# Kernel optimization log

Hardware: AMD Instinct MI355X
Metric: run time of the kernel (lower is better)

Reference implementation:

```python
import jax, jax.numpy as jnp
import numpy as np

EPS = 1e-4

def setup_inputs() -> dict:
    key = jax.random.key(0)
    x = jax.random.normal(key, (16, 256, 8192), dtype=jnp.float32)
    return {"x": x}

def reference(x):
    # x: [B, C, T]; cumulative (causal) normalization along time axis
    T = x.shape[-1]
    count = jnp.arange(1, T + 1, dtype=x.dtype).reshape(1, 1, T)
    cum_sum = jnp.cumsum(x, axis=-1)
    cum_pow_sum = jnp.cumsum(x * x, axis=-1)
    cum_mean = cum_sum / count
    cum_var = cum_pow_sum / count - cum_mean * cum_mean
    cum_std = jnp.sqrt(cum_var + EPS)
    return (x - cum_mean) / cum_std
```

## Files before the change

### kernel.cpp

```cpp
#include <hip/hip_runtime.h>

#define ROW_T   8192
#define THREADS 256
#define ITEMS   4
#define STILE   (THREADS * ITEMS)
#define NST     (ROW_T / STILE)
#define EPSV    1e-4f

__global__ __launch_bounds__(THREADS, 8)
void cumnorm_kernel(const float* __restrict__ x, float* __restrict__ out) {
    __shared__ float wbs[2][4];
    __shared__ float wbss[2][4];

    const int t    = threadIdx.x;
    const int lane = t & 63;
    const int wid  = t >> 6;

    const float* __restrict__ xr   = x   + (long long)blockIdx.x * ROW_T;
    float* __restrict__       outr = out + (long long)blockIdx.x * ROW_T;

    float carry_s = 0.f, carry_ss = 0.f;

    float4 cur = *reinterpret_cast<const float4*>(xr + t * ITEMS);
    float4 nxt;

    #pragma unroll
    for (int k = 0; k < NST; ++k) {
        if (k + 1 < NST)
            nxt = *reinterpret_cast<const float4*>(xr + (k + 1) * STILE + t * ITEMS);

        float s  = ((cur.x + cur.y) + (cur.z + cur.w));
        float ss = fmaf(cur.x, cur.x, fmaf(cur.y, cur.y,
                   fmaf(cur.z, cur.z, cur.w * cur.w)));

        float is = s, iss = ss;
        #pragma unroll
        for (int off = 1; off < 64; off <<= 1) {
            const float us  = __shfl_up(is, off);
            const float uss = __shfl_up(iss, off);
            if (lane >= off) { is += us; iss += uss; }
        }
        if (lane == 63) { wbs[k & 1][wid] = is; wbss[k & 1][wid] = iss; }
        __syncthreads();

        float cs = carry_s, css = carry_ss;
        #pragma unroll
        for (int w = 0; w < 4; ++w) {
            const float a = wbs[k & 1][w], b = wbss[k & 1][w];
            if (w < wid) { cs += a; css += b; }
            carry_s += a; carry_ss += b;
        }

        float S  = cs  + (is  - s);
        float SS = css + (iss - ss);

        const int e0 = k * STILE + t * ITEMS;
        float4 o;
        {
            const float v = cur.x; S += v; SS = fmaf(v, v, SS);
            const float inv = __builtin_amdgcn_rcpf((float)(e0 + 1));
            const float mean = S * inv;
            const float var  = fmaf(SS, inv, -(mean * mean));
            o.x = (v - mean) * __builtin_amdgcn_rsqf(var + EPSV);
        }
        {
            const float v = cur.y; S += v; SS = fmaf(v, v, SS);
            const float inv = __builtin_amdgcn_rcpf((float)(e0 + 2));
            const float mean = S * inv;
            const float var  = fmaf(SS, inv, -(mean * mean));
            o.y = (v - mean) * __builtin_amdgcn_rsqf(var + EPSV);
        }
        {
            const float v = cur.z; S += v; SS = fmaf(v, v, SS);
            const float inv = __builtin_amdgcn_rcpf((float)(e0 + 3));
            const float mean = S * inv;
            const float var  = fmaf(SS, inv, -(mean * mean));
            o.z = (v - mean) * __builtin_amdgcn_rsqf(var + EPSV);
        }
        {
            const float v = cur.w; S += v; SS = fmaf(v, v, SS);
            const float inv = __builtin_amdgcn_rcpf((float)(e0 + 4));
            const float mean = S * inv;
            const float var  = fmaf(SS, inv, -(mean * mean));
            o.w = (v - mean) * __builtin_amdgcn_rsqf(var + EPSV);
        }

        *reinterpret_cast<float4*>(outr + e0) = o;
        cur = nxt;
    }
}

extern "C" void kernel_launch(void* const* d_in, const int* in_sizes, int n_in,
                              void* d_out, int out_size, void* d_ws, size_t ws_size,
                              hipStream_t stream) {
    const float* x = (const float*)d_in[0];
    float* out = (float*)d_out;
    const int rows = out_size / ROW_T;
    cumnorm_kernel<<<rows, THREADS, 0, stream>>>(x, out);
}
```

Measured before the change: 229.4 us.

## Scan whole row in one pass with 1024-thread blocks and nontemporal stores

```diff
diff --git a/kernel.cpp b/kernel.cpp
--- a/kernel.cpp
+++ b/kernel.cpp
@@ -1,16 +1,17 @@
 #include <hip/hip_runtime.h>
 
 #define ROW_T   8192
-#define THREADS 256
-#define ITEMS   4
-#define STILE   (THREADS * ITEMS)
-#define NST     (ROW_T / STILE)
+#define THREADS 1024
+#define ITEMS   8
+#define NWAVES  (THREADS / 64)
 #define EPSV    1e-4f
+
+typedef float fvec4 __attribute__((ext_vector_type(4)));
 
 __global__ __launch_bounds__(THREADS, 8)
 void cumnorm_kernel(const float* __restrict__ x, float* __restrict__ out) {
-    __shared__ float wbs[2][4];
-    __shared__ float wbss[2][4];
+    __shared__ float wbs[NWAVES];
+    __shared__ float wbss[NWAVES];
 
     const int t    = threadIdx.x;
     const int lane = t & 63;
@@ -19,75 +20,55 @@
     const float* __restrict__ xr   = x   + (long long)blockIdx.x * ROW_T;
     float* __restrict__       outr = out + (long long)blockIdx.x * ROW_T;
 
-    float carry_s = 0.f, carry_ss = 0.f;
+    const int e0 = t * ITEMS;
 
-    float4 cur = *reinterpret_cast<const float4*>(xr + t * ITEMS);
-    float4 nxt;
+    const fvec4 va = *reinterpret_cast<const fvec4*>(xr + e0);
+    const fvec4 vb = *reinterpret_cast<const fvec4*>(xr + e0 + 4);
 
+    float s  = ((va.x + va.y) + (va.z + va.w)) + ((vb.x + vb.y) + (vb.z + vb.w));
+    float ss = fmaf(va.x, va.x, fmaf(va.y, va.y, fmaf(va.z, va.z, va.w * va.w)));
+    ss = fmaf(vb.x, vb.x, fmaf(vb.y, vb.y, fmaf(vb.z, vb.z, fmaf(vb.w, vb.w, ss))));
+
+    float is = s, iss = ss;
     #pragma unroll
-    for (int k = 0; k < NST; ++k) {
-        if (k + 1 < NST)
-            nxt = *reinterpret_cast<const float4*>(xr + (k + 1) * STILE + t * ITEMS);
+    for (int off = 1; off < 64; off <<= 1) {
+        const float us  = __shfl_up(is, off);
+        const float uss = __shfl_up(iss, off);
+        if (lane >= off) { is += us; iss += uss; }
+    }
+    if (lane == 63) { wbs[wid] = is; wbss[wid] = iss; }
+    __syncthreads();
 
-        float s  = ((cur.x + cur.y) + (cur.z + cur.w));
-        float ss = fmaf(cur.x, cur.x, fmaf(cur.y, cur.y,
-                   fmaf(cur.z, cur.z, cur.w * cur.w)));
+    float cs = 0.f, css = 0.f;
+    #pragma unroll
+    for (int w = 0; w < NWAVES; ++w) {
+        const float a = wbs[w], b = wbss[w];
+        if (w < wid) { cs += a; css += b; }
+    }
 
-        float is = s, iss = ss;
-        #pragma unroll
-        for (int off = 1; off < 64; off <<= 1) {
-            const float us  = __shfl_up(is, off);
-            const float uss = __shfl_up(iss, off);
-            if (lane >= off) { is += us; iss += uss; }
-        }
-        if (lane == 63) { wbs[k & 1][wid] = is; wbss[k & 1][wid] = iss; }
-        __syncthreads();
+    float S  = cs  + (is  - s);
+    float SS = css + (iss - ss);
 
-        float cs = carry_s, css = carry_ss;
-        #pragma unroll
-        for (int w = 0; w < 4; ++w) {
-            const float a = wbs[k & 1][w], b = wbss[k & 1][w];
-            if (w < wid) { cs += a; css += b; }
-            carry_s += a; carry_ss += b;
-        }
+    fvec4 o0, o1;
+#define CN_STEP(v, idx, dst) {                                            \
+        S += (v); SS = fmaf((v), (v), SS);                                \
+        const float inv  = __builtin_amdgcn_rcpf((float)(e0 + (idx) + 1));\
+        const float mean = S * inv;                                       \
+        const float var  = fmaf(SS, inv, -(mean * mean));                 \
+        (dst) = ((v) - mean) * __builtin_amdgcn_rsqf(var + EPSV);         \
+    }
+    CN_STEP(va.x, 0, o0.x)
+    CN_STEP(va.y, 1, o0.y)
+    CN_STEP(va.z, 2, o0.z)
+    CN_STEP(va.w, 3, o0.w)
+    CN_STEP(vb.x, 4, o1.x)
+    CN_STEP(vb.y, 5, o1.y)
+    CN_STEP(vb.z, 6, o1.z)
+    CN_STEP(vb.w, 7, o1.w)
+#undef CN_STEP
 
-        float S  = cs  + (is  - s);
-        float SS = css + (iss - ss);
-
-        const int e0 = k * STILE + t * ITEMS;
-        float4 o;
-        {
-            const float v = cur.x; S += v; SS = fmaf(v, v, SS);
-            const float inv = __builtin_amdgcn_rcpf((float)(e0 + 1));
-            const float mean = S * inv;
-            const float var  = fmaf(SS, inv, -(mean * mean));
-            o.x = (v - mean) * __builtin_amdgcn_rsqf(var + EPSV);
-        }
-        {
-            const float v = cur.y; S += v; SS = fmaf(v, v, SS);
-            const float inv = __builtin_amdgcn_rcpf((float)(e0 + 2));
-            const float mean = S * inv;
-            const float var  = fmaf(SS, inv, -(mean * mean));
-            o.y = (v - mean) * __builtin_amdgcn_rsqf(var + EPSV);
-        }
-        {
-            const float v = cur.z; S += v; SS = fmaf(v, v, SS);
-            const float inv = __builtin_amdgcn_rcpf((float)(e0 + 3));
-            const float mean = S * inv;
-            const float var  = fmaf(SS, inv, -(mean * mean));
-            o.z = (v - mean) * __builtin_amdgcn_rsqf(var + EPSV);
-        }
-        {
-            const float v = cur.w; S += v; SS = fmaf(v, v, SS);
-            const float inv = __builtin_amdgcn_rcpf((float)(e0 + 4));
-            const float mean = S * inv;
-            const float var  = fmaf(SS, inv, -(mean * mean));
-            o.w = (v - mean) * __builtin_amdgcn_rsqf(var + EPSV);
-        }
-
-        *reinterpret_cast<float4*>(outr + e0) = o;
-        cur = nxt;
-    }
+    __builtin_nontemporal_store(o0, reinterpret_cast<fvec4*>(outr + e0));
+    __builtin_nontemporal_store(o1, reinterpret_cast<fvec4*>(outr + e0 + 4));
 }
 
 extern "C" void kernel_launch(void* const* d_in, const int* in_sizes, int n_in,
```

Measured after the change: 236.6 us. +3.1%, slower.
